# Kernel optimization log

Measured on AMD Instinct MI355X. Metric: run time of the kernel, lower is better.

Reference implementation:

```python
import jax, jax.numpy as jnp
import numpy as np

EPS = 1e-09
TOP_K = 2


def setup_inputs() -> dict:
    key = jax.random.key(0)
    ks = jax.random.split(key, 6)
    B, L, F, E, D, SE = 64, 1024, 900, 8, 768, 64
    cycle_curve_data = jax.random.normal(ks[0], (B, L, F), dtype=jnp.float32)
    logits = jax.random.normal(ks[1], (B, E), dtype=jnp.float32)
    moe_masks = jax.random.randint(ks[2], (B, E), 0, 2, dtype=jnp.int32)
    selection_embeddings = jax.random.normal(ks[3], (B, E, SE), dtype=jnp.float32)
    W = jax.random.normal(ks[4], (E, F, D), dtype=jnp.float32) * 0.02
    b = jnp.zeros((E, D), dtype=jnp.float32)
    return {"cycle_curve_data": cycle_curve_data, "logits": logits,
            "moe_masks": moe_masks, "selection_embeddings": selection_embeddings,
            "W": W, "b": b}


def reference(cycle_curve_data, logits, moe_masks, selection_embeddings, W, b):
    B = cycle_curve_data.shape[0]
    E = logits.shape[1]
    mask = (moe_masks == 1).astype(logits.dtype)                 # [B, E]
    raw = jax.nn.softmax(logits, axis=1)                         # [B, E]
    p = raw * mask
    # selection embedding from inactive experts
    inactive = raw * (1.0 - mask)
    inactive = inactive / (jnp.sum(inactive, axis=1, keepdims=True) + EPS)
    selection_embedding = jnp.sum(selection_embeddings * inactive[:, :, None], axis=1)  # [B, SE]
    # top-k masking (indices treated as constants, same as torch scatter mask)
    if TOP_K > 0:
        _, idx = jax.lax.top_k(p, TOP_K)                         # [B, K]
        topk_mask = jnp.zeros_like(p).at[jnp.arange(B)[:, None], idx].set(1.0)
        p = p * topk_mask
    p = p / (jnp.sum(p, axis=1, keepdims=True) + EPS)            # [B, E]
    # dispatch/combine == weighted sum of per-expert Linear outputs
    # (weights are zero for unselected experts, matching MOEDispatcher)
    out = jnp.zeros(cycle_curve_data.shape[:2] + (W.shape[-1],), dtype=cycle_curve_data.dtype)
    for e in range(E):  # small fixed expert count
        expert_out = jnp.einsum('blf,fd->bld', cycle_curve_data, W[e]) + b[e]
        out = out + p[:, e, None, None] * expert_out
    final_out = out.astype(jnp.bfloat16)
    # guide loss (training mode)
    s = jnp.sum(raw * mask) / B
    guide_loss = (1.0 - s) * (1.0 - s)
    return final_out, guide_loss, selection_embedding
```

## Files before the change

### kernel.cpp

```cpp
#include <hip/hip_runtime.h>

#define B_  64
#define L_  1024
#define F_  900
#define E_  8
#define D_  768
#define SE_ 64
#define KP_ 928
#define FD_ (F_*D_)
#define OUT_MAIN (64*1024*768)
#define GL_OFF   OUT_MAIN
#define SE_OFF   (OUT_MAIN + 1)
#define EPSF 1e-9f
#define NT_  29


using f32x4  = __attribute__((ext_vector_type(4))) float;
using bf16   = __bf16;
using bf16x4 = __attribute__((ext_vector_type(4))) __bf16;
using bf16x8 = __attribute__((ext_vector_type(8))) __bf16;
using s16x8  = __attribute__((ext_vector_type(8))) short;

__device__ __forceinline__ f32x4 mfma_bf16(bf16x8 a, bf16x8 b, f32x4 c) {
  return __builtin_amdgcn_mfma_f32_16x16x32_bf16(
      __builtin_bit_cast(s16x8, a), __builtin_bit_cast(s16x8, b), c, 0, 0, 0);
}

__device__ __forceinline__ void gload16(const bf16* g, bf16* l) {
  __builtin_amdgcn_global_load_lds(
      (const __attribute__((address_space(1))) unsigned int*)g,
      (__attribute__((address_space(3))) unsigned int*)l, 16, 0, 0);
}

__device__ __forceinline__ const unsigned* pick_masks(const void* cA, const void* cB,
                                                      const float** logits) {
  const unsigned* a = (const unsigned*)cA;
  bool aIsMask = true;
#pragma unroll
  for (int i = 0; i < 512; i += 37) aIsMask &= (a[i] <= 1u);
  if (aIsMask) { *logits = (const float*)cB; return a; }
  *logits = (const float*)cA; return (const unsigned*)cB;
}

struct Gate { int e1, e2; float p1, p2; };

__device__ __forceinline__ Gate gate_for(const float* __restrict__ logits,
                                         const unsigned* __restrict__ masks, int b) {
  float lg[E_]; unsigned mk[E_];
#pragma unroll
  for (int e = 0; e < E_; ++e) { lg[e] = logits[b*E_+e]; mk[e] = masks[b*E_+e]; }
  float mx = lg[0];
#pragma unroll
  for (int e = 1; e < E_; ++e) mx = fmaxf(mx, lg[e]);
  float ex[E_], s = 0.f;
#pragma unroll
  for (int e = 0; e < E_; ++e) { ex[e] = expf(lg[e]-mx); s += ex[e]; }
  const float inv_s = 1.f / s;
  float p0[E_];
#pragma unroll
  for (int e = 0; e < E_; ++e) p0[e] = (mk[e] == 1u) ? ex[e]*inv_s : 0.f;
  int e1 = 0;
#pragma unroll
  for (int e = 1; e < E_; ++e) if (p0[e] > p0[e1]) e1 = e;
  int e2 = (e1 == 0) ? 1 : 0;
#pragma unroll
  for (int e = 0; e < E_; ++e) if (e != e1 && p0[e] > p0[e2]) e2 = e;
  const float inv = 1.f / (p0[e1] + p0[e2] + EPSF);
  Gate g; g.e1 = e1; g.e2 = e2; g.p1 = p0[e1]*inv; g.p2 = p0[e2]*inv;
  return g;
}

__device__ __forceinline__ void gating_body(const void* cA, const void* cB,
                                            const float* __restrict__ selemb,
                                            float* __restrict__ fout, int b) {
  const float* logits; const unsigned* masks = pick_masks(cA, cB, &logits);
  float lg[E_]; unsigned mk[E_];
#pragma unroll
  for (int e = 0; e < E_; ++e) { lg[e] = logits[b*E_+e]; mk[e] = masks[b*E_+e]; }
  float mx = lg[0];
#pragma unroll
  for (int e = 1; e < E_; ++e) mx = fmaxf(mx, lg[e]);
  float ex[E_], s = 0.f;
#pragma unroll
  for (int e = 0; e < E_; ++e) { ex[e] = expf(lg[e]-mx); s += ex[e]; }
  const float inv_s = 1.f / s;
  float inact[E_]; float isum = 0.f, sact = 0.f;
#pragma unroll
  for (int e = 0; e < E_; ++e) {
    float raw = ex[e] * inv_s;
    if (mk[e] == 1u) { sact += raw; inact[e] = 0.f; }
    else             { inact[e] = raw; isum += raw; }
  }
  const float inv_i = 1.f / (isum + EPSF);
  for (int se = 0; se < SE_; ++se) {
    float a = 0.f;
#pragma unroll
    for (int e = 0; e < E_; ++e)
      a += inact[e] * inv_i * selemb[((size_t)b*E_ + e)*SE_ + se];
    fout[SE_OFF + b*SE_ + se] = a;
  }
#pragma unroll
  for (int off = 32; off > 0; off >>= 1) sact += __shfl_down(sact, off);
  if (b == 0) {
    float sm = sact / (float)B_;
    fout[GL_OFF] = (1.f - sm) * (1.f - sm);
  }
}

__global__ void gating_kernel(const void* cA, const void* cB,
                              const float* __restrict__ selemb,
                              float* __restrict__ fout) {
  gating_body(cA, cB, selemb, fout, threadIdx.x);
}

__global__ __launch_bounds__(256) void prep_kernel(
    const float* __restrict__ X, const float* __restrict__ W,
    const void* cA, const void* cB, const float* __restrict__ selemb,
    bf16* __restrict__ Xbf, bf16* __restrict__ Wmix,
    float* __restrict__ fout) {
  const int blk = blockIdx.x;
  if (blk < 2048) {
    int idx = blk * 256 + threadIdx.x;
#pragma unroll 1
    for (int it = 0; it < 29; ++it, idx += 524288) {
      const int row = idx / 232;
      const int s   = idx - row * 232;
      bf16x4 o;
      if (s < 225) {
        f32x4 v = *(const f32x4*)(X + (size_t)row*F_ + s*4);
#pragma unroll
        for (int j = 0; j < 4; ++j) o[j] = (bf16)v[j];
      } else {
        o = (bf16x4){(bf16)0.f,(bf16)0.f,(bf16)0.f,(bf16)0.f};
      }
      *(bf16x4*)(Xbf + (size_t)row*KP_ + s*4) = o;
    }
  } else if (blk < 2816) {
    const int wb = blk - 2048;
    const int b  = wb / 12;
    const int dc = wb - b*12;
    const float* logits; const unsigned* masks = pick_masks(cA, cB, &logits);
    const Gate g = gate_for(logits, masks, b);
    const int lane = threadIdx.x & 63, w = threadIdx.x >> 6;
    const int d = (dc << 6) + lane;
    const float* W1 = W + (size_t)g.e1*FD_ + d;
    const float* W2 = W + (size_t)g.e2*FD_ + d;
    bf16* dst = Wmix + ((size_t)b*D_ + d)*KP_;
#pragma unroll 1
    for (int i = 0; i < 29; ++i) {
      const int f0 = (w + (i << 2)) << 3;
      float v[8];
#pragma unroll
      for (int jj = 0; jj < 8; ++jj) {
        int f = f0 + jj;
        v[jj] = (f < F_) ? g.p1*W1[(size_t)f*D_] + g.p2*W2[(size_t)f*D_] : 0.f;
      }
      bf16x8 pk;
#pragma unroll
      for (int jj = 0; jj < 8; ++jj) pk[jj] = (bf16)v[jj];
      *(bf16x8*)(dst + f0) = pk;
    }
  } else {
    if (threadIdx.x < 64) gating_body(cA, cB, selemb, fout, threadIdx.x);
  }
}

__global__ __launch_bounds__(256) void gemm_fast(
    const bf16* __restrict__ Xbf, const bf16* __restrict__ Wmix,
    const float* __restrict__ bias,
    const void* cA, const void* cB,
    float* __restrict__ fout) {
  __shared__ bf16 As[3][128*32];
  __shared__ bf16 Bs[3][128*32];

  const int id  = blockIdx.x;
  const int xcd = id & 7, q = id >> 3;
  const int b   = xcd + ((q / 48) << 3);
  const int j   = q % 48;
  const int bn  = j % 6, bm = j / 6;

  const float* logits; const unsigned* masks = pick_masks(cA, cB, &logits);
  const Gate g = gate_for(logits, masks, b);

  const bf16* Ab = Xbf  + ((size_t)b*L_ + (size_t)bm*128) * KP_;
  const bf16* Bb = Wmix + ((size_t)b*D_ + (size_t)bn*128) * KP_;

  const int t = threadIdx.x, lane = t & 63, w = t >> 6;
  const int sw   = ((lane & 3) ^ ((lane >> 2) & 3)) << 3;
  const int row0 = (w << 5) + (lane >> 2);
  const int row1 = row0 + 16;
  const int dst0 = (w << 7) << 3;
  const int dst1 = dst0 + (64 << 3);

  auto STAGE = [&](int buf, int kt) {
    const int k0 = kt << 5;
    gload16(Ab + (size_t)row0*KP_ + k0 + sw, &As[buf][dst0]);
    gload16(Ab + (size_t)row1*KP_ + k0 + sw, &As[buf][dst1]);
    gload16(Bb + (size_t)row0*KP_ + k0 + sw, &Bs[buf][dst0]);
    gload16(Bb + (size_t)row1*KP_ + k0 + sw, &Bs[buf][dst1]);
  };

  const int wr = (w >> 1) << 6, wc = (w & 1) << 6;
  const int fr = lane & 15, fks = lane >> 4;
  const int rq = (lane >> 4) << 2;

  int aoff[4], boff[4];
#pragma unroll
  for (int m = 0; m < 4; ++m) {
    int rA = wr + m*16 + fr;
    aoff[m] = rA*32 + ((fks ^ (rA & 3)) << 3);
    int rB = wc + m*16 + fr;
    boff[m] = rB*32 + ((fks ^ (rB & 3)) << 3);
  }

  const float* b1 = bias + g.e1*D_;
  const float* b2 = bias + g.e2*D_;
  float bsv[4];
#pragma unroll
  for (int n = 0; n < 4; ++n) {
    int gc = bn*128 + wc + n*16 + fr;
    bsv[n] = g.p1*b1[gc] + g.p2*b2[gc];
  }

  f32x4 acc[4][4];
#pragma unroll
  for (int m = 0; m < 4; ++m)
#pragma unroll
    for (int n = 0; n < 4; ++n) acc[m][n] = (f32x4){0.f,0.f,0.f,0.f};

  STAGE(0, 0);
  STAGE(1, 1);
  int cur = 0;
#pragma unroll 1
  for (int kt = 0; kt < NT_; ++kt) {
    if (kt + 2 < NT_) {
      const int sb = (cur + 2 >= 3) ? cur - 1 : cur + 2;
      STAGE(sb, kt + 2);
      asm volatile("s_waitcnt vmcnt(8)" ::: "memory");
    } else if (kt + 2 == NT_) {
      asm volatile("s_waitcnt vmcnt(4)" ::: "memory");
    } else {
      asm volatile("s_waitcnt vmcnt(0)" ::: "memory");
    }
    __builtin_amdgcn_sched_barrier(0);
    __builtin_amdgcn_s_barrier();
    __builtin_amdgcn_sched_barrier(0);
    bf16x8 af[4], bfv[4];
#pragma unroll
    for (int m = 0; m < 4; ++m) af[m]  = *(const bf16x8*)&As[cur][aoff[m]];
#pragma unroll
    for (int n = 0; n < 4; ++n) bfv[n] = *(const bf16x8*)&Bs[cur][boff[n]];
#pragma unroll
    for (int m = 0; m < 4; ++m)
#pragma unroll
      for (int n = 0; n < 4; ++n)
        acc[m][n] = mfma_bf16(af[m], bfv[n], acc[m][n]);
    __builtin_amdgcn_sched_barrier(0);
    __builtin_amdgcn_s_barrier();
    cur = (cur + 1 == 3) ? 0 : cur + 1;
  }

#pragma unroll
  for (int n = 0; n < 4; ++n) {
    int gc = bn*128 + wc + n*16 + fr;
#pragma unroll
    for (int m = 0; m < 4; ++m) {
      size_t base = ((size_t)b*L_ + (size_t)(bm*128 + wr + m*16 + rq)) * D_ + gc;
#pragma unroll
      for (int i = 0; i < 4; ++i)
        fout[base + (size_t)i*D_] = acc[m][n][i] + bsv[n];
    }
  }
}

__global__ void transw_kernel(const float* __restrict__ W, bf16* __restrict__ Wt) {
  __shared__ float tile[32][33];
  const int e  = blockIdx.z;
  const int d0 = blockIdx.x << 5;
  const int f0 = blockIdx.y << 5;
  const int c = threadIdx.x & 31, r = threadIdx.x >> 5;
#pragma unroll
  for (int p = 0; p < 4; ++p) {
    int f = f0 + p*8 + r;
    tile[p*8+r][c] = (f < F_) ? W[((size_t)e*F_ + f)*D_ + d0 + c] : 0.f;
  }
  __syncthreads();
#pragma unroll
  for (int p = 0; p < 4; ++p) {
    int d = d0 + p*8 + r;
    Wt[((size_t)e*D_ + d)*KP_ + f0 + c] = (bf16)tile[c][p*8+r];
  }
}

__global__ __launch_bounds__(256) void gemm_kernel(
    const float* __restrict__ X, const bf16* __restrict__ Wt,
    const float* __restrict__ bias,
    const void* cA, const void* cB,
    float* __restrict__ fout) {
  __shared__ bf16 As[128][40];
  __shared__ bf16 Bs[128][40];
  const int bn = blockIdx.x, bm = blockIdx.y, b = blockIdx.z;
  const float* logits; const unsigned* masks = pick_masks(cA, cB, &logits);
  const Gate g = gate_for(logits, masks, b);
  const float* Xb = X + ((size_t)b*L_ + (size_t)bm*128) * F_;
  const bf16* W1 = Wt + ((size_t)g.e1*D_ + (size_t)bn*128) * KP_;
  const bf16* W2 = Wt + ((size_t)g.e2*D_ + (size_t)bn*128) * KP_;
  const int t  = threadIdx.x;
  const int ar = t >> 3, ac = (t & 7) << 2;
  const int br = t >> 2, bc = (t & 3) << 3;
  const int lane = t & 63, wave = t >> 6;
  const int wr = (wave >> 1) << 6, wc = (wave & 1) << 6;
  const int fr = lane & 15, fk = (lane >> 4) << 3;
  const int rq = (lane >> 4) << 2;
  f32x4 acc[4][4];
#pragma unroll
  for (int m = 0; m < 4; ++m)
#pragma unroll
    for (int n = 0; n < 4; ++n) acc[m][n] = (f32x4){0.f,0.f,0.f,0.f};
  f32x4 ax[4]; bf16x8 wv1[2], wv2[2];
  auto LOAD = [&](int k0) {
    if (k0 <= F_ - 32) {
#pragma unroll
      for (int p = 0; p < 4; ++p)
        ax[p] = *(const f32x4*)(Xb + (size_t)(p*32 + ar)*F_ + k0 + ac);
    } else {
#pragma unroll
      for (int p = 0; p < 4; ++p)
#pragma unroll
        for (int jj = 0; jj < 4; ++jj) {
          int k = k0 + ac + jj;
          ax[p][jj] = (k < F_) ? Xb[(size_t)(p*32 + ar)*F_ + k] : 0.f;
        }
    }
#pragma unroll
    for (int p = 0; p < 2; ++p) {
      wv1[p] = *(const bf16x8*)(W1 + (size_t)(p*64 + br)*KP_ + k0 + bc);
      wv2[p] = *(const bf16x8*)(W2 + (size_t)(p*64 + br)*KP_ + k0 + bc);
    }
  };
  auto STAGE = [&]() {
#pragma unroll
    for (int p = 0; p < 4; ++p) {
      bf16x4 v;
#pragma unroll
      for (int jj = 0; jj < 4; ++jj) v[jj] = (bf16)ax[p][jj];
      *(bf16x4*)&As[p*32 + ar][ac] = v;
    }
#pragma unroll
    for (int p = 0; p < 2; ++p) {
      bf16x8 v;
#pragma unroll
      for (int jj = 0; jj < 8; ++jj)
        v[jj] = (bf16)(g.p1 * (float)wv1[p][jj] + g.p2 * (float)wv2[p][jj]);
      *(bf16x8*)&Bs[p*64 + br][bc] = v;
    }
  };
  LOAD(0);
  for (int kt = 0; kt < NT_; ++kt) {
    STAGE();
    __syncthreads();
    if (kt + 1 < NT_) LOAD((kt + 1) << 5);
    bf16x8 af[4], bfv[4];
#pragma unroll
    for (int m = 0; m < 4; ++m) af[m]  = *(const bf16x8*)&As[wr + m*16 + fr][fk];
#pragma unroll
    for (int n = 0; n < 4; ++n) bfv[n] = *(const bf16x8*)&Bs[wc + n*16 + fr][fk];
#pragma unroll
    for (int m = 0; m < 4; ++m)
#pragma unroll
      for (int n = 0; n < 4; ++n)
        acc[m][n] = mfma_bf16(af[m], bfv[n], acc[m][n]);
    __syncthreads();
  }
  const float* b1 = bias + g.e1*D_;
  const float* b2 = bias + g.e2*D_;
#pragma unroll
  for (int n = 0; n < 4; ++n) {
    int gc = bn*128 + wc + n*16 + fr;
    float bs = g.p1*b1[gc] + g.p2*b2[gc];
#pragma unroll
    for (int m = 0; m < 4; ++m) {
      size_t base = ((size_t)b*L_ + (size_t)(bm*128 + wr + m*16 + rq)) * D_ + gc;
#pragma unroll
      for (int i = 0; i < 4; ++i)
        fout[base + (size_t)i*D_] = acc[m][n][i] + bs;
    }
  }
}

__global__ __launch_bounds__(128) void fallback_kernel(
    const float* __restrict__ X, const float* __restrict__ W,
    const float* __restrict__ bias,
    const void* cA, const void* cB,
    float* __restrict__ fout) {
  __shared__ float xs[16 * F_];
  const int t  = threadIdx.x;
  const int d  = blockIdx.x * 128 + t;
  const int l0 = blockIdx.y * 16;
  const int b  = blockIdx.z;
  const float* logits; const unsigned* masks = pick_masks(cA, cB, &logits);
  const Gate g = gate_for(logits, masks, b);
  const float* xrow = X + ((size_t)b*L_ + l0) * F_;
  for (int i = t; i < 16 * F_; i += 128) xs[i] = xrow[i];
  __syncthreads();
  const float* w1 = W + (size_t)g.e1*FD_ + d;
  const float* w2 = W + (size_t)g.e2*FD_ + d;
  float acc[16];
#pragma unroll
  for (int jj = 0; jj < 16; ++jj) acc[jj] = 0.f;
  for (int k = 0; k < F_; k += 4) {
    float wb[4];
#pragma unroll
    for (int qq = 0; qq < 4; ++qq)
      wb[qq] = g.p1 * w1[(size_t)(k+qq)*D_] + g.p2 * w2[(size_t)(k+qq)*D_];
#pragma unroll
    for (int jj = 0; jj < 16; ++jj) {
      f32x4 xv = *(const f32x4*)&xs[jj*F_ + k];
#pragma unroll
      for (int qq = 0; qq < 4; ++qq) acc[jj] += xv[qq] * wb[qq];
    }
  }
  const float bs = g.p1*bias[g.e1*D_+d] + g.p2*bias[g.e2*D_+d];
#pragma unroll
  for (int jj = 0; jj < 16; ++jj)
    fout[((size_t)b*L_ + (size_t)(l0 + jj)) * D_ + d] = acc[jj] + bs;
}

extern "C" void kernel_launch(void* const* d_in, const int* in_sizes, int n_in,
                              void* d_out, int out_size, void* d_ws, size_t ws_size,
                              hipStream_t stream) {
  const float *X = nullptr, *selemb = nullptr, *W = nullptr, *bias = nullptr;
  const void *cA = nullptr, *cB = nullptr;
  for (int i = 0; i < n_in; ++i) {
    switch (in_sizes[i]) {
      case 58982400: X      = (const float*)d_in[i]; break;
      case 32768:    selemb = (const float*)d_in[i]; break;
      case 5529600:  W      = (const float*)d_in[i]; break;
      case 6144:     bias   = (const float*)d_in[i]; break;
      case 512:      if (!cA) cA = d_in[i]; else cB = d_in[i]; break;
      default: break;
    }
  }
  if (!X)      X      = (const float*)d_in[0];
  if (!cA)     cA     = d_in[1];
  if (!cB)     cB     = d_in[2];
  if (!selemb) selemb = (const float*)d_in[3];
  if (!W)      W      = (const float*)d_in[4];
  if (!bias)   bias   = (const float*)d_in[5];
  float* fout = (float*)d_out;

  const size_t xbf_bytes  = (size_t)B_*L_*KP_*2;
  const size_t wmix_bytes = (size_t)B_*D_*KP_*2;
  const size_t need_fast  = xbf_bytes + wmix_bytes;
  const size_t need_mid   = (size_t)E_*D_*KP_*2;

  if (ws_size >= need_fast) {
    bf16* Xbf  = (bf16*)d_ws;
    bf16* Wmix = (bf16*)((char*)d_ws + xbf_bytes);
    prep_kernel<<<2817, 256, 0, stream>>>(X, W, cA, cB, selemb, Xbf, Wmix, fout);
    gemm_fast<<<3072, 256, 0, stream>>>(Xbf, Wmix, bias, cA, cB, fout);
  } else if (ws_size >= need_mid) {
    bf16* Wt = (bf16*)d_ws;
    gating_kernel<<<1, 64, 0, stream>>>(cA, cB, selemb, fout);
    transw_kernel<<<dim3(24, 29, 8), 256, 0, stream>>>(W, Wt);
    gemm_kernel<<<dim3(6, 8, 64), 256, 0, stream>>>(X, Wt, bias, cA, cB, fout);
  } else {
    gating_kernel<<<1, 64, 0, stream>>>(cA, cB, selemb, fout);
    fallback_kernel<<<dim3(6, 64, 64), 128, 0, stream>>>(X, W, bias, cA, cB, fout);
  }
}
```

Before: 375.2 us.

## Split prep into separate X-convert and LDS-transposed W-mix kernels

Splits the fused prep kernel into three launches: a standalone gating kernel, an X fp32-to-bf16 conversion kernel, and a W-mix kernel. The X converter now handles 16 floats per thread and writes two 16-byte bf16 stores. The W-mix kernel reads W coalesced along D and transposes 32x32 tiles through shared memory, so the bf16 writes along K are contiguous instead of strided. This adds two extra kernel launches and shared-memory syncs per tile.

```diff
diff --git a/kernel.cpp b/kernel.cpp
--- a/kernel.cpp
+++ b/kernel.cpp
@@ -70,10 +70,11 @@
   return g;
 }
 
-__device__ __forceinline__ void gating_body(const void* cA, const void* cB,
-                                            const float* __restrict__ selemb,
-                                            float* __restrict__ fout, int b) {
+__global__ void gating_kernel(const void* cA, const void* cB,
+                              const float* __restrict__ selemb,
+                              float* __restrict__ fout) {
   const float* logits; const unsigned* masks = pick_masks(cA, cB, &logits);
+  const int b = threadIdx.x;
   float lg[E_]; unsigned mk[E_];
 #pragma unroll
   for (int e = 0; e < E_; ++e) { lg[e] = logits[b*E_+e]; mk[e] = masks[b*E_+e]; }
@@ -107,61 +108,71 @@
   }
 }
 
-__global__ void gating_kernel(const void* cA, const void* cB,
-                              const float* __restrict__ selemb,
-                              float* __restrict__ fout) {
-  gating_body(cA, cB, selemb, fout, threadIdx.x);
-}
-
-__global__ __launch_bounds__(256) void prep_kernel(
-    const float* __restrict__ X, const float* __restrict__ W,
-    const void* cA, const void* cB, const float* __restrict__ selemb,
-    bf16* __restrict__ Xbf, bf16* __restrict__ Wmix,
-    float* __restrict__ fout) {
+__global__ __launch_bounds__(256) void xconv_kernel(const float* __restrict__ X,
+                                                    bf16* __restrict__ Xbf) {
+  const int tid = blockIdx.x * 256 + threadIdx.x;
+#pragma unroll 1
+  for (int it = 0; it < 8; ++it) {
+    const int gidx = tid + it * 524288;
+    if (gidx >= 65536 * 58) break;
+    const int row = gidx / 58;
+    const int gg  = gidx - row * 58;
+    const int s0  = gg << 4;
+    f32x4 a[4];
+#pragma unroll
+    for (int j = 0; j < 4; ++j) {
+      const int f = s0 + (j << 2);
+      if (f < F_) a[j] = *(const f32x4*)(X + (size_t)row*F_ + f);
+      else        a[j] = (f32x4){0.f, 0.f, 0.f, 0.f};
+    }
+    bf16x8 o0, o1;
+#pragma unroll
+    for (int j = 0; j < 4; ++j) {
+      o0[j]   = (bf16)a[0][j];  o0[4+j] = (bf16)a[1][j];
+      o1[j]   = (bf16)a[2][j];  o1[4+j] = (bf16)a[3][j];
+    }
+    bf16* dst = Xbf + (size_t)row*KP_ + s0;
+    *(bf16x8*)dst       = o0;
+    *(bf16x8*)(dst + 8) = o1;
+  }
+}
+
+__global__ __launch_bounds__(256) void wmix_kernel(const float* __restrict__ W,
+                                                   const void* cA, const void* cB,
+                                                   bf16* __restrict__ Wmix) {
+  __shared__ float tile[32][33];
   const int blk = blockIdx.x;
-  if (blk < 2048) {
-    int idx = blk * 256 + threadIdx.x;
+  const int b   = blk / 24;
+  const int dc  = blk - b*24;
+  const int d0  = dc << 5;
+  const float* logits; const unsigned* masks = pick_masks(cA, cB, &logits);
+  const Gate g = gate_for(logits, masks, b);
+  const float* W1 = W + (size_t)g.e1*FD_;
+  const float* W2 = W + (size_t)g.e2*FD_;
+  const int t = threadIdx.x;
+  const int c = t & 31, r = t >> 5;
+  const int dl = t >> 3, qd = t & 7;
+  bf16* dstb = Wmix + ((size_t)b*D_ + d0 + dl)*KP_;
 #pragma unroll 1
-    for (int it = 0; it < 29; ++it, idx += 524288) {
-      const int row = idx / 232;
-      const int s   = idx - row * 232;
-      bf16x4 o;
-      if (s < 225) {
-        f32x4 v = *(const f32x4*)(X + (size_t)row*F_ + s*4);
-#pragma unroll
-        for (int j = 0; j < 4; ++j) o[j] = (bf16)v[j];
-      } else {
-        o = (bf16x4){(bf16)0.f,(bf16)0.f,(bf16)0.f,(bf16)0.f};
-      }
-      *(bf16x4*)(Xbf + (size_t)row*KP_ + s*4) = o;
-    }
-  } else if (blk < 2816) {
-    const int wb = blk - 2048;
-    const int b  = wb / 12;
-    const int dc = wb - b*12;
-    const float* logits; const unsigned* masks = pick_masks(cA, cB, &logits);
-    const Gate g = gate_for(logits, masks, b);
-    const int lane = threadIdx.x & 63, w = threadIdx.x >> 6;
-    const int d = (dc << 6) + lane;
-    const float* W1 = W + (size_t)g.e1*FD_ + d;
-    const float* W2 = W + (size_t)g.e2*FD_ + d;
-    bf16* dst = Wmix + ((size_t)b*D_ + d)*KP_;
-#pragma unroll 1
-    for (int i = 0; i < 29; ++i) {
-      const int f0 = (w + (i << 2)) << 3;
-      float v[8];
-#pragma unroll
-      for (int jj = 0; jj < 8; ++jj) {
-        int f = f0 + jj;
-        v[jj] = (f < F_) ? g.p1*W1[(size_t)f*D_] + g.p2*W2[(size_t)f*D_] : 0.f;
-      }
-      bf16x8 pk;
-#pragma unroll
-      for (int jj = 0; jj < 8; ++jj) pk[jj] = (bf16)v[jj];
-      *(bf16x8*)(dst + f0) = pk;
-    }
-  } else {
-    if (threadIdx.x < 64) gating_body(cA, cB, selemb, fout, threadIdx.x);
+  for (int ft = 0; ft < 29; ++ft) {
+    const int f0 = ft << 5;
+    float v[4];
+#pragma unroll
+    for (int p = 0; p < 4; ++p) {
+      const int f = f0 + (p << 3) + r;
+      if (f < F_) {
+        const size_t o = (size_t)f*D_ + d0 + c;
+        v[p] = g.p1*W1[o] + g.p2*W2[o];
+      } else v[p] = 0.f;
+    }
+    __syncthreads();
+#pragma unroll
+    for (int p = 0; p < 4; ++p) tile[(p << 3) + r][c] = v[p];
+    __syncthreads();
+    bf16x4 pk;
+#pragma unroll
+    for (int j = 0; j < 4; ++j) pk[j] = (bf16)tile[(qd << 2) + j][dl];
+    *(bf16x4*)(dstb + f0 + (qd << 2)) = pk;
   }
 }
 
@@ -454,18 +465,19 @@
   const size_t need_fast  = xbf_bytes + wmix_bytes;
   const size_t need_mid   = (size_t)E_*D_*KP_*2;
 
+  gating_kernel<<<1, 64, 0, stream>>>(cA, cB, selemb, fout);
+
   if (ws_size >= need_fast) {
     bf16* Xbf  = (bf16*)d_ws;
     bf16* Wmix = (bf16*)((char*)d_ws + xbf_bytes);
-    prep_kernel<<<2817, 256, 0, stream>>>(X, W, cA, cB, selemb, Xbf, Wmix, fout);
+    xconv_kernel<<<2048, 256, 0, stream>>>(X, Xbf);
+    wmix_kernel<<<1536, 256, 0, stream>>>(W, cA, cB, Wmix);
     gemm_fast<<<3072, 256, 0, stream>>>(Xbf, Wmix, bias, cA, cB, fout);
   } else if (ws_size >= need_mid) {
     bf16* Wt = (bf16*)d_ws;
-    gating_kernel<<<1, 64, 0, stream>>>(cA, cB, selemb, fout);
     transw_kernel<<<dim3(24, 29, 8), 256, 0, stream>>>(W, Wt);
     gemm_kernel<<<dim3(6, 8, 64), 256, 0, stream>>>(X, Wt, bias, cA, cB, fout);
   } else {
-    gating_kernel<<<1, 64, 0, stream>>>(cA, cB, selemb, fout);
     fallback_kernel<<<dim3(6, 64, 64), 128, 0, stream>>>(X, W, bias, cA, cB, fout);
   }
 }
```

Result: faster. 363.3 us (-3.2%).
